# Optimization experiments

Measured on AMD Instinct MI355X. Metric: run time of the kernel, lower is better.

## Reference

```python
import jax, jax.numpy as jnp
import numpy as np

N_NODES = 50000
N_EDGES = 800000
F_IN = 512
HIDDEN = 128
N_CLASSES = 40


def setup_inputs() -> dict:
    key = jax.random.key(0)
    ks = jax.random.split(key, 5)
    x = jax.random.normal(ks[0], (N_NODES, F_IN), dtype=jnp.float32)
    edge_index = jax.random.randint(ks[1], (2, N_EDGES), 0, N_NODES, dtype=jnp.int32)
    # Glorot-ish init for GCNConv linear weights, zero bias (PyG default bias=True)
    W1 = jax.random.normal(ks[2], (F_IN, HIDDEN), dtype=jnp.float32) * (1.0 / np.sqrt(F_IN))
    b1 = jnp.zeros((HIDDEN,), dtype=jnp.float32)
    W2 = jax.random.normal(ks[3], (HIDDEN, N_CLASSES), dtype=jnp.float32) * (1.0 / np.sqrt(HIDDEN))
    b2 = jnp.zeros((N_CLASSES,), dtype=jnp.float32)
    return {"x": x, "edge_index": edge_index, "W1": W1, "b1": b1, "W2": W2, "b2": b2}


def _gcn_conv(x, W, b, row, col, n_nodes):
    """PyG GCNConv: linear transform, then symmetric-normalized aggregation.

    row/col already include self-loops. deg computed over col (in-degree),
    norm = d^{-1/2}[row] * d^{-1/2}[col], out[row] += norm * h[col].
    """
    h = x @ W  # [N, out]
    ones = jnp.ones(col.shape[0], dtype=h.dtype)
    deg = jax.ops.segment_sum(ones, col, num_segments=n_nodes)  # >=1 due to self-loops
    dinv = jax.lax.rsqrt(deg)
    norm = dinv[row] * dinv[col]  # [E]
    msgs = h[col] * norm[:, None]  # [E, out] gather + scale
    out = jax.ops.segment_sum(msgs, row, num_segments=n_nodes)  # scatter-add
    return out + b


def reference(x, edge_index, W1, b1, W2, b2):
    n = x.shape[0]
    loop = jnp.arange(n, dtype=edge_index.dtype)
    row = jnp.concatenate([edge_index[0], loop])
    col = jnp.concatenate([edge_index[1], loop])
    h = _gcn_conv(x, W1, b1, row, col, n)
    h = jax.nn.relu(h)
    # dropout with training=False is identity (eval-mode reference)
    out = _gcn_conv(h, W2, b2, row, col, n)
    return out
```

## Files before the change

kernel.cpp:

```cpp
#include <hip/hip_runtime.h>
#include <hip/hip_bf16.h>

#define N_NODES 50000
#define N_EDGES 800000
#define F_IN 512
#define HIDDEN 128
#define N_CLASSES 40
#define NSCAN 196

typedef __attribute__((ext_vector_type(4))) float f32x4;
typedef __attribute__((ext_vector_type(8))) short s16x8;

__device__ __forceinline__ unsigned bf16r(float f) {
    unsigned u = __float_as_uint(f);
    return (u + 0x7fffu + ((u >> 16) & 1u)) >> 16;
}
__device__ __forceinline__ unsigned pkbf(float lo, float hi) {
    return bf16r(lo) | (bf16r(hi) << 16);
}
__device__ __forceinline__ float bflo(unsigned u) { return __uint_as_float(u << 16); }
__device__ __forceinline__ float bfhi(unsigned u) { return __uint_as_float(u & 0xffff0000u); }

__global__ void prep_kernel(const float* __restrict__ W1, const float* __restrict__ W2,
                            uint4* __restrict__ w1f, uint4* __restrict__ w2f) {
    int f = blockIdx.x * 256 + threadIdx.x;
    if (f < 8192) {
        int lane = f & 63, u = (f >> 6) & 7, c = f >> 9;
        int k0 = c * 32 + ((lane >> 4) << 3), n = u * 16 + (lane & 15);
        float v[8];
        #pragma unroll
        for (int j = 0; j < 8; ++j) v[j] = W1[(size_t)(k0 + j) * HIDDEN + n];
        uint4 o;
        o.x = pkbf(v[0], v[1]); o.y = pkbf(v[2], v[3]);
        o.z = pkbf(v[4], v[5]); o.w = pkbf(v[6], v[7]);
        w1f[f] = o;
    } else if (f < 8960) {
        int g = f - 8192;
        int lane = g & 63, u = (g >> 6) % 3, c = g / 192;
        int k0 = c * 32 + ((lane >> 4) << 3), n = u * 16 + (lane & 15);
        float v[8];
        #pragma unroll
        for (int j = 0; j < 8; ++j)
            v[j] = (n < N_CLASSES) ? W2[(size_t)(k0 + j) * N_CLASSES + n] : 0.0f;
        uint4 o;
        o.x = pkbf(v[0], v[1]); o.y = pkbf(v[2], v[3]);
        o.z = pkbf(v[4], v[5]); o.w = pkbf(v[6], v[7]);
        w2f[g] = o;
    }
}

__global__ __launch_bounds__(256) void fused_kernel(
    const float* __restrict__ x, const uint4* __restrict__ w1f,
    unsigned short* __restrict__ h1s,
    const int* __restrict__ row, const int* __restrict__ col,
    int* __restrict__ rowcnt, int* __restrict__ colcnt, int* __restrict__ pos8)
{
    __shared__ uint4 XAf[256];
    const int q = blockIdx.x / 5, rm = blockIdx.x % 5;

    if (rm != 0) {
        const int cb = q * 4 + rm - 1;
        const int e = cb * 256 + threadIdx.x;
        if (e < N_EDGES) {
            pos8[e] = atomicAdd(&rowcnt[row[e]], 1);
            atomicAdd(&colcnt[col[e]], 1);
        }
        return;
    }

    const int tid  = threadIdx.x;
    const int wave = tid >> 6, lane = tid & 63;
    const int l16  = lane & 15, quad = lane >> 4;
    const int row0 = q * 64;

    f32x4 acc[4][2] = {};

    int sr = row0 + wave * 16 + l16;
    if (sr >= N_NODES) sr = N_NODES - 1;
    const float* xrow = x + (size_t)sr * F_IN + (quad << 3);

    for (int c = 0; c < F_IN / 32; ++c) {
        float4 a = *(const float4*)(xrow + c * 32);
        float4 b = *(const float4*)(xrow + c * 32 + 4);
        uint4 fr;
        fr.x = pkbf(a.x, a.y); fr.y = pkbf(a.z, a.w);
        fr.z = pkbf(b.x, b.y); fr.w = pkbf(b.z, b.w);
        XAf[tid] = fr;
        __syncthreads();

        uint4 t0 = w1f[(size_t)(c * 8 + wave * 2 + 0) * 64 + lane];
        uint4 t1 = w1f[(size_t)(c * 8 + wave * 2 + 1) * 64 + lane];
        s16x8 bf0 = *(s16x8*)&t0, bf1 = *(s16x8*)&t1;

        #pragma unroll
        for (int i = 0; i < 4; ++i) {
            uint4 ta = XAf[i * 64 + lane];
            s16x8 af = *(s16x8*)&ta;
            acc[i][0] = __builtin_amdgcn_mfma_f32_16x16x32_bf16(af, bf0, acc[i][0], 0, 0, 0);
            acc[i][1] = __builtin_amdgcn_mfma_f32_16x16x32_bf16(af, bf1, acc[i][1], 0, 0, 0);
        }
        __syncthreads();
    }

    const int n0 = wave * 32;
    #pragma unroll
    for (int i = 0; i < 4; ++i) {
        #pragma unroll
        for (int p = 0; p < 4; ++p) {
            int gr = row0 + i * 16 + quad * 4 + p;
            if (gr < N_NODES) {
                #pragma unroll
                for (int u = 0; u < 2; ++u)
                    h1s[(size_t)gr * HIDDEN + n0 + u * 16 + l16] =
                        (unsigned short)bf16r(acc[i][u][p]);
            }
        }
    }
}

__global__ void scan_blocks_kernel(const int* __restrict__ rowcnt,
                                   const int* __restrict__ colcnt,
                                   float* __restrict__ dinv,
                                   int* __restrict__ rowptr, int* __restrict__ partials) {
    __shared__ int s[256];
    const int tid = threadIdx.x;
    const int i = blockIdx.x * 256 + tid;
    const int v = (i < N_NODES) ? rowcnt[i] : 0;
    s[tid] = v;
    __syncthreads();
    #pragma unroll
    for (int off = 1; off < 256; off <<= 1) {
        int t = (tid >= off) ? s[tid - off] : 0;
        __syncthreads();
        s[tid] += t;
        __syncthreads();
    }
    if (i < N_NODES) {
        rowptr[i] = s[tid] - v;
        dinv[i] = rsqrtf(1.0f + (float)colcnt[i]);
    }
    if (tid == 255) partials[blockIdx.x] = s[255];
}

__global__ void scan_partials_kernel(int* __restrict__ partials) {
    __shared__ int s[256];
    const int tid = threadIdx.x;
    const int v = (tid < NSCAN) ? partials[tid] : 0;
    s[tid] = v;
    __syncthreads();
    #pragma unroll
    for (int off = 1; off < 256; off <<= 1) {
        int t = (tid >= off) ? s[tid - off] : 0;
        __syncthreads();
        s[tid] += t;
        __syncthreads();
    }
    if (tid < NSCAN) partials[tid] = s[tid] - v;
}

__global__ void scan_add_kernel(int* __restrict__ rowptr, const int* __restrict__ partials) {
    int i = blockIdx.x * 256 + threadIdx.x;
    if (i < N_NODES) rowptr[i] += partials[blockIdx.x];
    if (i == 0) rowptr[N_NODES] = N_EDGES;
}

__global__ void place_kernel(const int* __restrict__ row, const int* __restrict__ col,
                             const int* __restrict__ rowptr, const int* __restrict__ pos8,
                             int* __restrict__ ecol) {
    int e = blockIdx.x * 256 + threadIdx.x;
    if (e < N_EDGES) ecol[rowptr[row[e]] + pos8[e]] = col[e];
}

__global__ __launch_bounds__(256) void gather1_kernel(
    const int* __restrict__ rowptr, const int* __restrict__ ecol,
    const float* __restrict__ dinv, const unsigned* __restrict__ h1u,
    const float* __restrict__ b1, unsigned* __restrict__ agg1u)
{
    const int wave = threadIdx.x >> 6, lane = threadIdx.x & 63;
    const int r = blockIdx.x * 4 + wave;
    if (r >= N_NODES) return;
    const int start = rowptr[r], end = rowptr[r + 1];

    float ax = 0.f, ay = 0.f, bx = 0.f, by = 0.f;
    float cx = 0.f, cy = 0.f, dx = 0.f, dy = 0.f;
    int e = start;
    for (; e + 3 < end; e += 4) {
        const int c0 = ecol[e], c1 = ecol[e + 1], c2 = ecol[e + 2], c3 = ecol[e + 3];
        const float d0 = dinv[c0], d1 = dinv[c1], d2 = dinv[c2], d3 = dinv[c3];
        unsigned u0 = h1u[(size_t)c0 * 64 + lane];
        unsigned u1 = h1u[(size_t)c1 * 64 + lane];
        unsigned u2 = h1u[(size_t)c2 * 64 + lane];
        unsigned u3 = h1u[(size_t)c3 * 64 + lane];
        ax = fmaf(bflo(u0), d0, ax); ay = fmaf(bfhi(u0), d0, ay);
        bx = fmaf(bflo(u1), d1, bx); by = fmaf(bfhi(u1), d1, by);
        cx = fmaf(bflo(u2), d2, cx); cy = fmaf(bfhi(u2), d2, cy);
        dx = fmaf(bflo(u3), d3, dx); dy = fmaf(bfhi(u3), d3, dy);
    }
    for (; e < end; ++e) {
        const int c = ecol[e];
        const float d = dinv[c];
        unsigned u = h1u[(size_t)c * 64 + lane];
        ax = fmaf(bflo(u), d, ax); ay = fmaf(bfhi(u), d, ay);
    }
    const float s = dinv[r];
    unsigned us = h1u[(size_t)r * 64 + lane];
    float sx = (ax + bx) + (cx + dx) + bflo(us) * s;
    float sy = (ay + by) + (cy + dy) + bfhi(us) * s;
    const float2 bb = *(const float2*)&b1[lane * 2];
    float ox = fmaxf(fmaf(s, sx, bb.x), 0.f);
    float oy = fmaxf(fmaf(s, sy, bb.y), 0.f);
    agg1u[(size_t)r * 64 + lane] = pkbf(ox, oy);
}

__global__ __launch_bounds__(256) void gemm2_kernel(
    const uint4* __restrict__ agg1q, const uint4* __restrict__ w2f,
    const float* __restrict__ dinv, float* __restrict__ h2s)
{
    __shared__ uint4 XAf[512];
    const int tid  = threadIdx.x;
    const int wave = tid >> 6, lane = tid & 63;
    const int l16  = lane & 15, quad = lane >> 4;
    const int row0 = blockIdx.x * 128;

    f32x4 acc[2][3] = {};

    int r1 = row0 + wave * 16 + l16;        if (r1 >= N_NODES) r1 = N_NODES - 1;
    int r2 = row0 + (4 + wave) * 16 + l16;  if (r2 >= N_NODES) r2 = N_NODES - 1;

    for (int c = 0; c < 4; ++c) {
        XAf[tid]       = agg1q[(size_t)r1 * 16 + c * 4 + quad];
        XAf[tid + 256] = agg1q[(size_t)r2 * 16 + c * 4 + quad];
        __syncthreads();

        s16x8 bf[3];
        #pragma unroll
        for (int u = 0; u < 3; ++u) {
            uint4 t = w2f[(size_t)(c * 3 + u) * 64 + lane];
            bf[u] = *(s16x8*)&t;
        }
        #pragma unroll
        for (int i = 0; i < 2; ++i) {
            uint4 ta = XAf[(wave * 2 + i) * 64 + lane];
            s16x8 af = *(s16x8*)&ta;
            #pragma unroll
            for (int u = 0; u < 3; ++u)
                acc[i][u] = __builtin_amdgcn_mfma_f32_16x16x32_bf16(af, bf[u], acc[i][u], 0, 0, 0);
        }
        __syncthreads();
    }

    #pragma unroll
    for (int i = 0; i < 2; ++i) {
        #pragma unroll
        for (int p = 0; p < 4; ++p) {
            int gr = row0 + (wave * 2 + i) * 16 + quad * 4 + p;
            if (gr < N_NODES) {
                float s = dinv[gr];
                #pragma unroll
                for (int u = 0; u < 3; ++u) {
                    int ncol = u * 16 + l16;
                    if (ncol < N_CLASSES)
                        h2s[(size_t)gr * N_CLASSES + ncol] = acc[i][u][p] * s;
                }
            }
        }
    }
}

__global__ __launch_bounds__(256) void gather2_kernel(
    const int* __restrict__ rowptr, const int* __restrict__ ecol,
    const float* __restrict__ dinv, const float* __restrict__ h2s,
    const float* __restrict__ b2, float* __restrict__ out)
{
    const int wave = threadIdx.x >> 6, lane = threadIdx.x & 63;
    const int r = blockIdx.x * 4 + wave;
    if (r >= N_NODES || lane >= N_CLASSES) return;
    const int start = rowptr[r], end = rowptr[r + 1];

    float a0 = 0.f, a1 = 0.f, a2 = 0.f, a3 = 0.f;
    int e = start;
    for (; e + 3 < end; e += 4) {
        a0 += h2s[(size_t)ecol[e] * N_CLASSES + lane];
        a1 += h2s[(size_t)ecol[e + 1] * N_CLASSES + lane];
        a2 += h2s[(size_t)ecol[e + 2] * N_CLASSES + lane];
        a3 += h2s[(size_t)ecol[e + 3] * N_CLASSES + lane];
    }
    for (; e < end; ++e) a0 += h2s[(size_t)ecol[e] * N_CLASSES + lane];
    float s = (a0 + a1) + (a2 + a3) + h2s[(size_t)r * N_CLASSES + lane];
    out[(size_t)r * N_CLASSES + lane] = fmaf(dinv[r], s, b2[lane]);
}

extern "C" void kernel_launch(void* const* d_in, const int* in_sizes, int n_in,
                              void* d_out, int out_size, void* d_ws, size_t ws_size,
                              hipStream_t stream)
{
    const float* x  = (const float*)d_in[0];
    const int*   ei = (const int*)d_in[1];
    const float* W1 = (const float*)d_in[2];
    const float* b1 = (const float*)d_in[3];
    const float* W2 = (const float*)d_in[4];
    const float* b2 = (const float*)d_in[5];
    const int* row = ei;
    const int* col = ei + N_EDGES;

    float* ws = (float*)d_ws;
    int*   rowcnt   = (int*)(ws);
    int*   colcnt   = (int*)(ws + 65536);
    float* dinv     = ws + 131072;
    int*   rowptr   = (int*)(ws + 196608);
    int*   partials = (int*)(ws + 262144);
    int*   pos8     = (int*)(ws + 270336);
    int*   ecol     = (int*)(ws + 1089536);
    uint4* w1f      = (uint4*)(ws + 1908736);
    uint4* w2f      = (uint4*)(ws + 1941504);
    unsigned short* h1s = (unsigned short*)(ws + 1944576);
    unsigned*       h1u = (unsigned*)h1s;
    unsigned* agg1u = (unsigned*)(ws + 5144576);
    uint4*    agg1q = (uint4*)agg1u;
    float*    h2s   = ws + 8344576;
    float*    out   = (float*)d_out;

    hipMemsetAsync(rowcnt, 0, 2 * 65536 * sizeof(int), stream);
    prep_kernel<<<35, 256, 0, stream>>>(W1, W2, w1f, w2f);

    fused_kernel<<<3910, 256, 0, stream>>>(x, w1f, h1s, row, col, rowcnt, colcnt, pos8);

    scan_blocks_kernel<<<NSCAN, 256, 0, stream>>>(rowcnt, colcnt, dinv, rowptr, partials);
    scan_partials_kernel<<<1, 256, 0, stream>>>(partials);
    scan_add_kernel<<<NSCAN, 256, 0, stream>>>(rowptr, partials);
    place_kernel<<<3125, 256, 0, stream>>>(row, col, rowptr, pos8, ecol);

    gather1_kernel<<<N_NODES / 4, 256, 0, stream>>>(rowptr, ecol, dinv, h1u, b1, agg1u);
    gemm2_kernel<<<(N_NODES + 127) / 128, 256, 0, stream>>>(agg1q, w2f, dinv, h2s);
    gather2_kernel<<<N_NODES / 4, 256, 0, stream>>>(rowptr, ecol, dinv, h2s, b2, out);
}
```

Before: 329.7 us.

## Store layer-2 features in bf16, repack gathers, merge scan kernels and regroup edge-count blocks

Layer-2 transformed features are now stored as bf16 pairs, and gather2 uses three lane groups of 20 that each read a different neighbor and combine results with shuffles. This halves gather traffic and uses more lanes of each wave. Gather1 drops its scalar tail loop for a clamped, masked 4-wide loop. The partials-scan kernel is removed, and each scan_add block now reduces its preceding partials itself. The edge-counting blocks in the fused kernel are reduced to 391, each handling eight edges per thread. The cost is extra bf16 rounding of the layer-2 features and redundant partial reductions across scan_add blocks.

```diff
diff --git a/kernel.cpp b/kernel.cpp
--- a/kernel.cpp
+++ b/kernel.cpp
@@ -7,6 +7,7 @@
 #define HIDDEN 128
 #define N_CLASSES 40
 #define NSCAN 196
+#define CB 391
 
 typedef __attribute__((ext_vector_type(4))) float f32x4;
 typedef __attribute__((ext_vector_type(8))) short s16x8;
@@ -56,18 +57,21 @@
     int* __restrict__ rowcnt, int* __restrict__ colcnt, int* __restrict__ pos8)
 {
     __shared__ uint4 XAf[256];
-    const int q = blockIdx.x / 5, rm = blockIdx.x % 5;
-
-    if (rm != 0) {
-        const int cb = q * 4 + rm - 1;
-        const int e = cb * 256 + threadIdx.x;
-        if (e < N_EDGES) {
-            pos8[e] = atomicAdd(&rowcnt[row[e]], 1);
-            atomicAdd(&colcnt[col[e]], 1);
+
+    if (blockIdx.x < CB) {
+        const int t = blockIdx.x * 256 + threadIdx.x;
+        #pragma unroll
+        for (int j = 0; j < 8; ++j) {
+            const int e = t + j * (CB * 256);
+            if (e < N_EDGES) {
+                pos8[e] = atomicAdd(&rowcnt[row[e]], 1);
+                atomicAdd(&colcnt[col[e]], 1);
+            }
         }
         return;
     }
 
+    const int q = blockIdx.x - CB;
     const int tid  = threadIdx.x;
     const int wave = tid >> 6, lane = tid & 63;
     const int l16  = lane & 15, quad = lane >> 4;
@@ -142,25 +146,19 @@
     if (tid == 255) partials[blockIdx.x] = s[255];
 }
 
-__global__ void scan_partials_kernel(int* __restrict__ partials) {
+__global__ void scan_add_kernel(int* __restrict__ rowptr, const int* __restrict__ partials) {
     __shared__ int s[256];
     const int tid = threadIdx.x;
-    const int v = (tid < NSCAN) ? partials[tid] : 0;
-    s[tid] = v;
+    s[tid] = (tid < blockIdx.x) ? partials[tid] : 0;
     __syncthreads();
     #pragma unroll
-    for (int off = 1; off < 256; off <<= 1) {
-        int t = (tid >= off) ? s[tid - off] : 0;
-        __syncthreads();
-        s[tid] += t;
-        __syncthreads();
-    }
-    if (tid < NSCAN) partials[tid] = s[tid] - v;
-}
-
-__global__ void scan_add_kernel(int* __restrict__ rowptr, const int* __restrict__ partials) {
-    int i = blockIdx.x * 256 + threadIdx.x;
-    if (i < N_NODES) rowptr[i] += partials[blockIdx.x];
+    for (int off = 128; off > 0; off >>= 1) {
+        if (tid < off) s[tid] += s[tid + off];
+        __syncthreads();
+    }
+    const int base = s[0];
+    const int i = blockIdx.x * 256 + tid;
+    if (i < N_NODES) rowptr[i] += base;
     if (i == 0) rowptr[N_NODES] = N_EDGES;
 }
 
@@ -183,24 +181,23 @@
 
     float ax = 0.f, ay = 0.f, bx = 0.f, by = 0.f;
     float cx = 0.f, cy = 0.f, dx = 0.f, dy = 0.f;
-    int e = start;
-    for (; e + 3 < end; e += 4) {
-        const int c0 = ecol[e], c1 = ecol[e + 1], c2 = ecol[e + 2], c3 = ecol[e + 3];
-        const float d0 = dinv[c0], d1 = dinv[c1], d2 = dinv[c2], d3 = dinv[c3];
-        unsigned u0 = h1u[(size_t)c0 * 64 + lane];
-        unsigned u1 = h1u[(size_t)c1 * 64 + lane];
-        unsigned u2 = h1u[(size_t)c2 * 64 + lane];
-        unsigned u3 = h1u[(size_t)c3 * 64 + lane];
-        ax = fmaf(bflo(u0), d0, ax); ay = fmaf(bfhi(u0), d0, ay);
-        bx = fmaf(bflo(u1), d1, bx); by = fmaf(bfhi(u1), d1, by);
-        cx = fmaf(bflo(u2), d2, cx); cy = fmaf(bfhi(u2), d2, cy);
-        dx = fmaf(bflo(u3), d3, dx); dy = fmaf(bfhi(u3), d3, dy);
-    }
-    for (; e < end; ++e) {
-        const int c = ecol[e];
-        const float d = dinv[c];
-        unsigned u = h1u[(size_t)c * 64 + lane];
-        ax = fmaf(bflo(u), d, ax); ay = fmaf(bfhi(u), d, ay);
+    if (start < end) {
+        for (int e = start; e < end; e += 4) {
+            const int i1 = min(e + 1, end - 1), i2 = min(e + 2, end - 1), i3 = min(e + 3, end - 1);
+            const int c0 = ecol[e], c1 = ecol[i1], c2 = ecol[i2], c3 = ecol[i3];
+            const float d0 = dinv[c0];
+            const float d1 = (e + 1 < end) ? dinv[c1] : 0.f;
+            const float d2 = (e + 2 < end) ? dinv[c2] : 0.f;
+            const float d3 = (e + 3 < end) ? dinv[c3] : 0.f;
+            unsigned u0 = h1u[(size_t)c0 * 64 + lane];
+            unsigned u1 = h1u[(size_t)c1 * 64 + lane];
+            unsigned u2 = h1u[(size_t)c2 * 64 + lane];
+            unsigned u3 = h1u[(size_t)c3 * 64 + lane];
+            ax = fmaf(bflo(u0), d0, ax); ay = fmaf(bfhi(u0), d0, ay);
+            bx = fmaf(bflo(u1), d1, bx); by = fmaf(bfhi(u1), d1, by);
+            cx = fmaf(bflo(u2), d2, cx); cy = fmaf(bfhi(u2), d2, cy);
+            dx = fmaf(bflo(u3), d3, dx); dy = fmaf(bfhi(u3), d3, dy);
+        }
     }
     const float s = dinv[r];
     unsigned us = h1u[(size_t)r * 64 + lane];
@@ -214,7 +211,7 @@
 
 __global__ __launch_bounds__(256) void gemm2_kernel(
     const uint4* __restrict__ agg1q, const uint4* __restrict__ w2f,
-    const float* __restrict__ dinv, float* __restrict__ h2s)
+    const float* __restrict__ dinv, unsigned short* __restrict__ h2b)
 {
     __shared__ uint4 XAf[512];
     const int tid  = threadIdx.x;
@@ -260,7 +257,8 @@
                 for (int u = 0; u < 3; ++u) {
                     int ncol = u * 16 + l16;
                     if (ncol < N_CLASSES)
-                        h2s[(size_t)gr * N_CLASSES + ncol] = acc[i][u][p] * s;
+                        h2b[(size_t)gr * N_CLASSES + ncol] =
+                            (unsigned short)bf16r(acc[i][u][p] * s);
                 }
             }
         }
@@ -269,25 +267,37 @@
 
 __global__ __launch_bounds__(256) void gather2_kernel(
     const int* __restrict__ rowptr, const int* __restrict__ ecol,
-    const float* __restrict__ dinv, const float* __restrict__ h2s,
+    const float* __restrict__ dinv, const unsigned* __restrict__ h2u,
     const float* __restrict__ b2, float* __restrict__ out)
 {
     const int wave = threadIdx.x >> 6, lane = threadIdx.x & 63;
     const int r = blockIdx.x * 4 + wave;
-    if (r >= N_NODES || lane >= N_CLASSES) return;
+    if (r >= N_NODES) return;
+    const int g = lane / 20;
+    const int j = lane - g * 20;
     const int start = rowptr[r], end = rowptr[r + 1];
 
-    float a0 = 0.f, a1 = 0.f, a2 = 0.f, a3 = 0.f;
-    int e = start;
-    for (; e + 3 < end; e += 4) {
-        a0 += h2s[(size_t)ecol[e] * N_CLASSES + lane];
-        a1 += h2s[(size_t)ecol[e + 1] * N_CLASSES + lane];
-        a2 += h2s[(size_t)ecol[e + 2] * N_CLASSES + lane];
-        a3 += h2s[(size_t)ecol[e + 3] * N_CLASSES + lane];
-    }
-    for (; e < end; ++e) a0 += h2s[(size_t)ecol[e] * N_CLASSES + lane];
-    float s = (a0 + a1) + (a2 + a3) + h2s[(size_t)r * N_CLASSES + lane];
-    out[(size_t)r * N_CLASSES + lane] = fmaf(dinv[r], s, b2[lane]);
+    float sx = 0.f, sy = 0.f;
+    if (g < 3 && start < end) {
+        for (int e = start; e < end; e += 3) {
+            const int ee = e + g;
+            const int c = ecol[min(ee, end - 1)];
+            unsigned u = h2u[(size_t)c * 20 + j];
+            u = (ee < end) ? u : 0u;
+            sx += bflo(u); sy += bfhi(u);
+        }
+    }
+    float tx = sx + __shfl(sx, lane + 20, 64) + __shfl(sx, lane + 40, 64);
+    float ty = sy + __shfl(sy, lane + 20, 64) + __shfl(sy, lane + 40, 64);
+    if (lane < 20) {
+        unsigned us = h2u[(size_t)r * 20 + j];
+        tx += bflo(us); ty += bfhi(us);
+        const float2 bb = *(const float2*)&b2[2 * j];
+        float2 o;
+        o.x = fmaf(dinv[r], tx, bb.x);
+        o.y = fmaf(dinv[r], ty, bb.y);
+        *(float2*)&out[(size_t)r * N_CLASSES + 2 * j] = o;
+    }
 }
 
 extern "C" void kernel_launch(void* const* d_in, const int* in_sizes, int n_in,
@@ -317,20 +327,20 @@
     unsigned*       h1u = (unsigned*)h1s;
     unsigned* agg1u = (unsigned*)(ws + 5144576);
     uint4*    agg1q = (uint4*)agg1u;
-    float*    h2s   = ws + 8344576;
+    unsigned short* h2b = (unsigned short*)(ws + 8344576);
+    unsigned*       h2u = (unsigned*)h2b;
     float*    out   = (float*)d_out;
 
     hipMemsetAsync(rowcnt, 0, 2 * 65536 * sizeof(int), stream);
     prep_kernel<<<35, 256, 0, stream>>>(W1, W2, w1f, w2f);
 
-    fused_kernel<<<3910, 256, 0, stream>>>(x, w1f, h1s, row, col, rowcnt, colcnt, pos8);
+    fused_kernel<<<CB + 782, 256, 0, stream>>>(x, w1f, h1s, row, col, rowcnt, colcnt, pos8);
 
     scan_blocks_kernel<<<NSCAN, 256, 0, stream>>>(rowcnt, colcnt, dinv, rowptr, partials);
-    scan_partials_kernel<<<1, 256, 0, stream>>>(partials);
     scan_add_kernel<<<NSCAN, 256, 0, stream>>>(rowptr, partials);
     place_kernel<<<3125, 256, 0, stream>>>(row, col, rowptr, pos8, ecol);
 
     gather1_kernel<<<N_NODES / 4, 256, 0, stream>>>(rowptr, ecol, dinv, h1u, b1, agg1u);
-    gemm2_kernel<<<(N_NODES + 127) / 128, 256, 0, stream>>>(agg1q, w2f, dinv, h2s);
-    gather2_kernel<<<N_NODES / 4, 256, 0, stream>>>(rowptr, ecol, dinv, h2s, b2, out);
-}
+    gemm2_kernel<<<(N_NODES + 127) / 128, 256, 0, stream>>>(agg1q, w2f, dinv, h2b);
+    gather2_kernel<<<N_NODES / 4, 256, 0, stream>>>(rowptr, ecol, dinv, h2u, b2, out);
+}
```

After: 332.1 us. About the same (+0.7%).
